# Optimization experiments

Measured on AMD Instinct MI355X. Metric: run time of the kernel, lower is better.

Reference implementation:

```python
import jax, jax.numpy as jnp
import numpy as np

B, L, P = 65536, 512, 96
E_LIN, E = 14, 16
FFT = 512
TEMP = 0.07
K = 2
EPS = 1e-5


def setup_inputs() -> dict:
    key = jax.random.key(0)
    k0, k1, k2 = jax.random.split(key, 3)
    x = jax.random.normal(k0, (B, L), dtype=jnp.float32)
    Wg = jax.random.normal(k1, (E, FFT // 2), dtype=jnp.float32) * 0.02
    bg = jnp.zeros((E,), dtype=jnp.float32)
    Wr = jax.random.normal(k2, (E_LIN, P, L), dtype=jnp.float32) * 0.02
    br = jnp.zeros((E_LIN, P), dtype=jnp.float32)
    return {"x": x, "Wg": Wg, "bg": bg, "Wr": Wr, "br": br}


def _periodogram(x):
    # x: [B, L] -> normalized power spectrum [B, FFT//2]
    x0 = x - jnp.mean(x, axis=1, keepdims=True)
    dft = jnp.fft.fft(x0, n=FFT, axis=1) / np.float32(np.sqrt(FFT))
    dft = dft[:, : FFT // 2]
    I = dft.real ** 2 + dft.imag ** 2
    s = jnp.sum(I, axis=1, keepdims=True)
    s = jnp.where(s == 0, jnp.ones_like(s), s)
    return I / s


def reference(x, Wg, bg, Wr, br):
    # gating (eval mode: no noise, divide by temperature)
    I = _periodogram(x)                                  # [B, F/2]
    gate = (I @ Wg.T + bg) / TEMP                        # [B, E]
    topv, topi = jax.lax.top_k(gate, K)                  # [B, K]
    gates = jax.nn.softmax(topv, axis=1)                 # [B, K]

    # RLinear experts: RevIN(norm) -> Linear -> RevIN(denorm); stats detached
    mu = jax.lax.stop_gradient(jnp.mean(x, axis=1, keepdims=True))        # [B,1]
    sd = jax.lax.stop_gradient(jnp.sqrt(jnp.var(x, axis=1, keepdims=True) + EPS))
    xn = (x - mu) / sd                                   # [B, L]
    yr = jnp.einsum('bl,epl->bep', xn, Wr) + br          # [B, E_LIN, P]
    yr = yr * sd[:, :, None] + mu[:, :, None]

    mean_out = jnp.broadcast_to(jnp.mean(x, axis=1, keepdims=True), (x.shape[0], P))[:, None, :]
    naive_out = jnp.broadcast_to(x[:, -1:], (x.shape[0], P))[:, None, :]

    eo = jnp.concatenate([yr, mean_out, naive_out], axis=1)   # [B, E, P]
    sel = jnp.take_along_axis(eo, topi[:, :, None], axis=1)   # [B, K, P]
    out = jnp.sum(gates[:, :, None] * sel, axis=1)            # [B, P]
    return out
```

## Files before the change

### kernel.cpp

```cpp
#include <hip/hip_runtime.h>
#include <math.h>

#define NB_B 65536
#define NL   512
#define NP   96
#define NE   16
#define NEL  14
#define NF   256
#define TEMP_INV (1.0f/0.07f)
#define TAU  1e-5f
#define PI_D 3.14159265358979323846
#define MAXCHK 1536

typedef __attribute__((ext_vector_type(8))) short bf16x8;
typedef __attribute__((ext_vector_type(4))) float f32x4;
typedef __attribute__((ext_vector_type(4))) unsigned int u32x4;


#define WS_PCNT     0
#define WS_HOLES    16384
#define WS_PBASE    32768
#define WS_FLAGCNT  33792
#define WS_NCHK     33824
#define WS_HOLECNT  33840
#define WS_FLAG     33856
#define WS_SSUM     296000
#define WS_WGT      301376
#define WS_BGT      317760
#define WS_TWD      319872
#define WS_REC      328064
#define WS_HDR      590208
#define WS_RIDX     1638784
#define WS_WRB      1933696
#define WS_DESC     3506560
#define WS_XB16     3512704
#define WS_XB16_END 70621568

__device__ __forceinline__ unsigned short f2bf(float f) {
    unsigned u = __float_as_uint(f);
    unsigned r = (u + 0x7fffu + ((u >> 16) & 1u)) >> 16;
    return (unsigned short)r;
}
__device__ __forceinline__ bf16x8 ldnt_bf16x8(const unsigned short* p) {
    u32x4 v = __builtin_nontemporal_load((const u32x4*)p);
    union { u32x4 u; bf16x8 h; } c; c.u = v; return c.h;
}
__device__ __forceinline__ float4 ldnt_f4(const float4* p) {
    u32x4 v = __builtin_nontemporal_load((const u32x4*)p);
    union { u32x4 u; float4 f; } c; c.u = v; return c.f;
}

__global__ __launch_bounds__(256) void k_prep(
    const float* __restrict__ Wg, const float* __restrict__ bg,
    const float* __restrict__ Wr,
    float* __restrict__ Ssum, float* __restrict__ WgE, float* __restrict__ bgT,
    double2* __restrict__ twd,
    int* __restrict__ pcnt, int* __restrict__ flagcnt, int* __restrict__ holecnt,
    ushort4* __restrict__ Wrb, int perm)
{
    int g = blockIdx.x * 256 + threadIdx.x;
    {
        ushort4 o = make_ushort4(0, 0, 0, 0);
        if (g < NEL * NP * NL / 4) {
            float4 v;
            if (perm) {
                int row = g >> 7, sq = g & 127;
                int ll = sq >> 1, kb = (sq & 1) * 4;
                const float* wr = Wr + (size_t)row * NL + ll;
                v.x = wr[(kb + 0) * 64]; v.y = wr[(kb + 1) * 64];
                v.z = wr[(kb + 2) * 64]; v.w = wr[(kb + 3) * 64];
            } else {
                v = ((const float4*)Wr)[g];
            }
            o.x = f2bf(v.x); o.y = f2bf(v.y); o.z = f2bf(v.z); o.w = f2bf(v.w);
        }
        Wrb[g] = o;
    }
    if (g < NEL * NP * 8) {
        int row = g >> 3, seg = g & 7;
        const float4* w = (const float4*)(Wr + (size_t)row * NL + seg * 64);
        float s = 0.f;
#pragma unroll
        for (int i = 0; i < 16; i++) { float4 v = w[i]; s += v.x + v.y + v.z + v.w; }
        s += __shfl_xor(s, 1); s += __shfl_xor(s, 2); s += __shfl_xor(s, 4);
        if (seg == 0) Ssum[row] = s;
    }
    if (g < 4096) {
        int c = g & 3, e = (g >> 2) & 15, f4 = g >> 6;
        WgE[g] = Wg[e * NF + f4 * 4 + c] * TEMP_INV;
    }
    if (g < 512) {
        double a = -2.0 * PI_D * (double)g / 512.0;
        twd[g] = make_double2(cos(a), sin(a));
    }
    if (g < 256) pcnt[g << 4] = 0;
    if (g < NE) bgT[g] = bg[g] * TEMP_INV;
    if (g == 300) *flagcnt = 0;
    if (g == 301) *holecnt = 0;
}

__global__ __launch_bounds__(256, 4) void k_gate(
    const float* __restrict__ x,
    const float4* __restrict__ WgE4, const float* __restrict__ bgT,
    int* __restrict__ rec, float4* __restrict__ hdr,
    int* __restrict__ flaglist, int* __restrict__ flagcnt,
    int* __restrict__ pcnt, unsigned short* __restrict__ xb16)
{
    __shared__ __align__(16) float2 s_z[4][576];
    float* s_Iv = (float*)&s_z[0][0];

    const int t = threadIdx.x;
    const int wv = t >> 6, l = t & 63;
    const int b0 = blockIdx.x * 8 + wv * 2;

    const float th = -6.283185307179586f / 512.0f;
    const float R2 = 0.70710678118654752f;
    float s1, c1; __sincosf((float)l * th, &s1, &c1);
    float s2, c2; __sincosf((float)(2 * l) * th, &s2, &c2);
    float sw0, cw0; __sincosf((float)((l & 31) << 3) * th, &sw0, &cw0);
    float sw1, cw1; __sincosf((float)((l & 15) << 4) * th, &sw1, &cw1);
    float sw2, cw2; __sincosf((float)((l & 7) << 5) * th, &sw2, &cw2);
    float2 tw0[4];
    tw0[0] = make_float2(c1, s1);
    tw0[1] = make_float2(R2 * (c1 + s1), R2 * (s1 - c1));
    tw0[2] = make_float2(s1, -c1);
    tw0[3] = make_float2(tw0[1].y, -tw0[1].x);
    float2 tw1[2];
    tw1[0] = make_float2(c2, s2);
    tw1[1] = make_float2(s2, -c2);
    const float2 w2 = make_float2(c2 * c2 - s2 * s2, 2.f * c2 * s2);
    float2 wst[5];
    wst[0] = make_float2(cw0, sw0);
    wst[1] = make_float2(cw1, sw1);
    wst[2] = make_float2(cw2, sw2);
    {
        int j2 = l & 3;
        float cc3 = (j2 == 0) ? 1.f : (j2 == 1) ? R2 : (j2 == 2) ? 0.f : -R2;
        float ss3 = (j2 == 0) ? 0.f : (j2 == 2) ? -1.f : -R2;
        wst[3] = make_float2(cc3, ss3);
    }
    wst[4] = (l & 1) ? make_float2(0.f, -1.f) : make_float2(1.f, 0.f);

    const float* xa = x + (size_t)b0 * NL;
    const float* xb = xa + NL;
    float xr[8], xi[8];
#pragma unroll
    for (int k = 0; k < 8; k++) { xr[k] = xa[k * 64 + l]; xi[k] = xb[k * 64 + l]; }
    const float last_a = __shfl(xr[7], 63);
    const float last_b = __shfl(xi[7], 63);

    if (xb16) {
        unsigned pa_[4], pb_[4];
#pragma unroll
        for (int j = 0; j < 4; j++) {
            asm("v_cvt_pk_bf16_f32 %0, %1, %2" : "=v"(pa_[j]) : "v"(xr[2 * j]), "v"(xr[2 * j + 1]));
            asm("v_cvt_pk_bf16_f32 %0, %1, %2" : "=v"(pb_[j]) : "v"(xi[2 * j]), "v"(xi[2 * j + 1]));
        }
        *(uint4*)(xb16 + (size_t)b0 * NL + l * 8)       = *(uint4*)pa_;
        *(uint4*)(xb16 + (size_t)(b0 + 1) * NL + l * 8) = *(uint4*)pb_;
    }

#pragma unroll
    for (int k = 0; k < 4; k++) {
        float2 w = tw0[k];
        float ur = xr[k], ui = xi[k], vr = xr[k + 4], vi = xi[k + 4];
        xr[k] = ur + vr; xi[k] = ui + vi;
        float dr = ur - vr, di = ui - vi;
        xr[k + 4] = dr * w.x - di * w.y; xi[k + 4] = dr * w.y + di * w.x;
    }
    {
        const int kk[4] = {0, 1, 4, 5};
#pragma unroll
        for (int g2 = 0; g2 < 4; g2++) {
            int k = kk[g2];
            float2 w = tw1[k & 1];
            float ur = xr[k], ui = xi[k], vr = xr[k + 2], vi = xi[k + 2];
            xr[k] = ur + vr; xi[k] = ui + vi;
            float dr = ur - vr, di = ui - vi;
            xr[k + 2] = dr * w.x - di * w.y; xi[k + 2] = dr * w.y + di * w.x;
        }
    }
    {
#pragma unroll
        for (int k = 0; k < 8; k += 2) {
            float ur = xr[k], ui = xi[k], vr = xr[k + 1], vi = xi[k + 1];
            xr[k] = ur + vr; xi[k] = ui + vi;
            float dr = ur - vr, di = ui - vi;
            xr[k + 1] = dr * w2.x - di * w2.y; xi[k + 1] = dr * w2.y + di * w2.x;
        }
    }
#pragma unroll
    for (int st = 3; st < 8; st++) {
        const int half = 256 >> st;
        const float2 w = wst[st - 3];
        const bool up = (l & half) != 0;
        const float sg = up ? -1.f : 1.f;
        const float cc = up ? w.x : 1.f;
        const float ss = up ? w.y : 0.f;
#pragma unroll
        for (int k = 0; k < 8; k++) {
            float pr = __shfl_xor(xr[k], half);
            float pi = __shfl_xor(xi[k], half);
            float tr = fmaf(sg, xr[k], pr);
            float ti = fmaf(sg, xi[k], pi);
            xr[k] = tr * cc - ti * ss;
            xi[k] = tr * ss + ti * cc;
        }
    }
    {
        const float sg = (l & 1) ? -1.f : 1.f;
#pragma unroll
        for (int k = 0; k < 8; k++) {
            float pr = __shfl_xor(xr[k], 1);
            float pi = __shfl_xor(xi[k], 1);
            xr[k] = fmaf(sg, xr[k], pr);
            xi[k] = fmaf(sg, xi[k], pi);
        }
    }

#pragma unroll
    for (int k = 0; k < 8; k++) {
        int i = k * 64 + l;
        s_z[wv][i + (i >> 3)] = make_float2(xr[k], xi[k]);
    }

    float Ia[4], Ib[4];
    float psa = 0.f, psb = 0.f;
#pragma unroll
    for (int j = 0; j < 4; j++) {
        int f = (l << 2) | j;
        int i1_ = (int)(__brev((unsigned)f) >> 23);
        int i2_ = (int)(__brev((unsigned)((512 - f) & 511)) >> 23);
        float2 z1 = s_z[wv][i1_ + (i1_ >> 3)];
        float2 z2 = s_z[wv][i2_ + (i2_ >> 3)];
        float pr_ = z1.x + z2.x, qm = z1.y - z2.y;
        float qp = z1.y + z2.y, pm = z1.x - z2.x;
        float va = pr_ * pr_ + qm * qm;
        float vb = qp * qp + pm * pm;
        if (f == 0) { va = 0.f; vb = 0.f; }
        Ia[j] = va; Ib[j] = vb;
        psa += va; psb += vb;
    }
#pragma unroll
    for (int m = 1; m < 64; m <<= 1) {
        psa += __shfl_xor(psa, m); psb += __shfl_xor(psb, m);
    }
    const float psa_raw = psa, psb_raw = psb;
    if (psa == 0.f) psa = 1.f;
    if (psb == 0.f) psb = 1.f;
    const float inv_a = 1.f / psa, inv_b = 1.f / psb;

    const float2 Z0   = s_z[wv][0];
    const float2 Z256 = s_z[wv][1];

    float* wI = s_Iv + wv * 1152;
    const int io = (l << 2) + ((l >> 4) << 2);
    *(float4*)(wI + io)       = make_float4(Ia[0], Ia[1], Ia[2], Ia[3]);
    *(float4*)(wI + 272 + io) = make_float4(Ib[0], Ib[1], Ib[2], Ib[3]);

    const int e16 = l & 15, cq = l >> 4;
    const float bgv = bgT[e16];
    float accA = 0.f, accB = 0.f;
    const float* rA = wI + cq * 68;
    const float* rB = rA + 272;
#pragma unroll 4
    for (int jj = 0; jj < 16; jj++) {
        float4 ia = *(const float4*)(rA + 4 * jj);
        float4 ib = *(const float4*)(rB + 4 * jj);
        float4 w = WgE4[(cq * 16 + jj) * 16 + e16];
        accA += ia.x * w.x + ia.y * w.y + ia.z * w.z + ia.w * w.w;
        accB += ib.x * w.x + ib.y * w.y + ib.z * w.z + ib.w * w.w;
    }
    accA += __shfl_xor(accA, 16); accA += __shfl_xor(accA, 32);
    accB += __shfl_xor(accB, 16); accB += __shfl_xor(accB, 32);

    float v = ((l & 16) ? accB * inv_b : accA * inv_a) + bgv;

    float b0v = v; int b0i = e16;
#pragma unroll
    for (int m = 1; m < 16; m <<= 1) {
        float ov = __shfl_xor(b0v, m); int oi = __shfl_xor(b0i, m);
        if (ov > b0v || (ov == b0v && oi < b0i)) { b0v = ov; b0i = oi; }
    }
    float v1 = (e16 == b0i) ? -1e30f : v;
    float b1v = v1; int b1i = e16;
#pragma unroll
    for (int m = 1; m < 16; m <<= 1) {
        float ov = __shfl_xor(b1v, m); int oi = __shfl_xor(b1i, m);
        if (ov > b1v || (ov == b1v && oi < b1i)) { b1v = ov; b1i = oi; }
    }
    float v2 = (e16 == b1i) ? -1e30f : v1;
    float b2v = v2;
#pragma unroll
    for (int m = 1; m < 16; m <<= 1) {
        float ov = __shfl_xor(b2v, m);
        b2v = fmaxf(b2v, ov);
    }

    if (l == 0 || l == 16) {
        const int r = l >> 4;
        const int b = b0 + r;
        const float mu = (r ? Z0.y : Z0.x) * (1.f / 512.f);
        const float Jv = r ? Z256.y : Z256.x;
        const float ps = r ? psb_raw : psa_raw;
        const float sd = sqrtf((0.5f * ps + Jv * Jv) * (1.f / 262144.f) + 1e-5f);
        const float last = r ? last_b : last_a;
        const float w0 = 1.f / (1.f + expf(b1v - b0v));
        const int pid = b0i * 16 + b1i;
        const int lo = atomicAdd(&pcnt[pid << 4], 1);
        rec[b] = (pid << 24) | lo;
        hdr[b] = make_float4(mu, sd, last, w0);
        if (b1v - b2v < TAU) {
            int pos = atomicAdd(flagcnt, 1);
            flaglist[pos] = b;
        }
    }
}

__global__ __launch_bounds__(256) void k_refine(
    const float* __restrict__ x, const double2* __restrict__ twd,
    const float* __restrict__ Wg, const float* __restrict__ bg,
    int* __restrict__ rec, float4* __restrict__ hdr,
    const int* __restrict__ flaglist, const int* __restrict__ flagcnt,
    int* __restrict__ pcnt, int* __restrict__ holes, int* __restrict__ holecnt)
{
    __shared__ double s_x[512];
    __shared__ double s_I[256];
    __shared__ double s_red[16];
    __shared__ double s_g[16];
    const int nf = *flagcnt;
    const int t = threadIdx.x;
    const int wid = t >> 6, lane = t & 63;
    for (int fi = blockIdx.x; fi < nf; fi += gridDim.x) {
        const int b = flaglist[fi];
        const float* xp = x + (size_t)b * NL;
        double v0 = (double)xp[t], v1 = (double)xp[t + 256];
        double lsum = v0 + v1;
        for (int m = 1; m < 64; m <<= 1) lsum += __shfl_xor(lsum, m);
        if (lane == 0) s_red[wid] = lsum;
        __syncthreads();
        double mu = (s_red[0] + s_red[1] + s_red[2] + s_red[3]) * (1.0 / 512.0);
        s_x[t] = v0 - mu; s_x[t + 256] = v1 - mu;
        __syncthreads();
        double2 w = twd[t];
        double pr = 1.0, pi = 0.0, cr = 0.0, ci = 0.0;
        for (int n = 0; n < 512; n++) {
            double xv = s_x[n];
            cr += xv * pr; ci += xv * pi;
            double t2 = pr * w.x - pi * w.y;
            pi = pr * w.y + pi * w.x;
            pr = t2;
        }
        double I = cr * cr + ci * ci;
        s_I[t] = I;
        double ls = I;
        for (int m = 1; m < 64; m <<= 1) ls += __shfl_xor(ls, m);
        if (lane == 0) s_red[8 + wid] = ls;
        __syncthreads();
        double stot = s_red[8] + s_red[9] + s_red[10] + s_red[11];
        if (stot == 0.0) stot = 1.0;
        if (t < 16) {
            double acc = 0.0;
            const float* wrow = Wg + t * NF;
            for (int f = 0; f < NF; f++) acc += s_I[f] * (double)wrow[f];
            s_g[t] = (acc / stot + (double)bg[t]) * (1.0 / 0.07);
        }
        __syncthreads();
        if (t == 0) {
            double c0 = -1e300, c1 = -1e300; int j0 = 0, j1 = 0;
            for (int i = 0; i < 16; i++) {
                double v = s_g[i];
                if (v > c0) { c1 = c0; j1 = j0; c0 = v; j0 = i; }
                else if (v > c1) { c1 = v; j1 = i; }
            }
            double e1 = exp(c1 - c0);
            float w0f = (float)(1.0 / (1.0 + e1));
            int newpid = j0 * 16 + j1;
            int oldrec = rec[b];
            int oldpid = (int)(((unsigned)oldrec) >> 24);
            if (newpid == oldpid) {
                ((float*)(hdr + b))[3] = w0f;
            } else {
                int pos = atomicAdd(holecnt, 1);
                if (pos < 4096) {
                    int nlo = atomicAdd(&pcnt[newpid << 4], 1);
                    rec[b] = (newpid << 24) | nlo;
                    holes[pos] = oldrec;
                    ((float*)(hdr + b))[3] = w0f;
                }
            }
        }
        __syncthreads();
    }
}

__global__ __launch_bounds__(256) void k_scan(
    const int* __restrict__ pcnt, int* __restrict__ pbase,
    int* __restrict__ desc, int* __restrict__ nchk)
{
    __shared__ int s[256], c[256];
    const int t = threadIdx.x;
    const int n = pcnt[t << 4];
    s[t] = n;
    c[t] = (n + 63) >> 6;
    __syncthreads();
    for (int off = 1; off < 256; off <<= 1) {
        int v1 = (t >= off) ? s[t - off] : 0;
        int v2 = (t >= off) ? c[t - off] : 0;
        __syncthreads();
        s[t] += v1; c[t] += v2;
        __syncthreads();
    }
    int excl = t ? s[t - 1] : 0;
    int cexcl = t ? c[t - 1] : 0;
    pbase[t] = excl;
    int myc = (n + 63) >> 6;
    for (int j = 0; j < myc; j++) desc[cexcl + j] = (t << 16) | j;
    if (t == 255) *nchk = cexcl + myc;
}

__global__ __launch_bounds__(256) void k_scatter(
    const int* __restrict__ rec, const int* __restrict__ pbase,
    int* __restrict__ ridx,
    const int* __restrict__ holes, const int* __restrict__ holecnt)
{
    const int t = threadIdx.x;
    const int b = blockIdx.x * 256 + t;
    unsigned v = (unsigned)rec[b];
    ridx[pbase[v >> 24] + (v & 0xFFFFFF)] = b;
    if (blockIdx.x == 0) {
        int nh = *holecnt; if (nh > 4096) nh = 4096;
        for (int h = t; h < nh; h += 256) {
            unsigned hv = (unsigned)holes[h];
            ridx[pbase[hv >> 24] + (hv & 0xFFFFFF)] = -1;
        }
    }
}

__global__ __launch_bounds__(256) void k_gemm3(
    const unsigned short* __restrict__ xb16,
    const unsigned short* __restrict__ Wrb,
    const float* __restrict__ br, const float* __restrict__ Ssum,
    const float4* __restrict__ hdr, float* __restrict__ out,
    const int* __restrict__ pcnt, const int* __restrict__ pbase,
    const int* __restrict__ ridx,
    const int* __restrict__ desc, const int* __restrict__ nchk)
{
    __shared__ __align__(16) unsigned short sB[2][96 * 68];
    __shared__ int    s_idx[64];
    __shared__ float4 s_hdr[64];
    __shared__ float  s_br[2][96], s_S[2][96];
    const int lb = (int)(blockIdx.x % 8) * (MAXCHK / 8) + (int)(blockIdx.x / 8);
    if (lb >= *nchk) return;
    const int d = desc[lb];
    const int pid = d >> 16, cc = d & 0xffff;
    const int n = pcnt[pid << 4];
    const int base = pbase[pid];
    const int i0 = pid >> 4, i1 = pid & 15;
    const int t = threadIdx.x;
    const int lane = t & 63, wv = t >> 6;
    const int quad = lane >> 4, l16 = lane & 15;
    if (t < 96) {
        s_br[0][t] = (i0 < NEL) ? br[i0 * NP + t] : 0.f;
        s_S [0][t] = (i0 < NEL) ? Ssum[i0 * NP + t] : 0.f;
        s_br[1][t] = (i1 < NEL) ? br[i1 * NP + t] : 0.f;
        s_S [1][t] = (i1 < NEL) ? Ssum[i1 * NP + t] : 0.f;
    }
    if (t < 64) {
        int g = cc * 64 + t;
        bool vld = g < n;
        int row = vld ? ridx[base + g] : -1;
        s_idx[t] = row;
        s_hdr[t] = (row >= 0) ? ldnt_f4(hdr + row) : make_float4(0.f, 0.f, 0.f, 0.f);
    }

    const unsigned short* wb[2];
    wb[0] = Wrb + (size_t)i0 * NP * NL;
    wb[1] = Wrb + (size_t)i1 * NP * NL;
    unsigned boff[6]; int bpos[6], bex[6];
#pragma unroll
    for (int it = 0; it < 6; it++) {
        int ex = (it >= 3);
        int fl = t + (it - 3 * ex) * 256;
        int p = fl >> 3, kg = fl & 7;
        bex[it] = ex;
        boff[it] = (unsigned)(p * NL + kg * 8);
        bpos[it] = p * 68 + kg * 8;
    }

    bf16x8 bR[6];
#pragma unroll
    for (int it = 0; it < 6; it++) bR[it] = *(const bf16x8*)(wb[bex[it]] + boff[it]);
    __syncthreads();

    int arow = s_idx[wv * 16 + l16]; if (arow < 0) arow = 0;
    const unsigned short* aP = xb16 + (size_t)arow * NL + quad * 8;

    f32x4 acc[2][6];
#pragma unroll
    for (int ex = 0; ex < 2; ex++)
#pragma unroll
        for (int j = 0; j < 6; j++) acc[ex][j] = (f32x4){0.f, 0.f, 0.f, 0.f};

    bf16x8 a0 = ldnt_bf16x8(aP);
    bf16x8 a1 = ldnt_bf16x8(aP + 32);

    for (int kb = 0; kb < NL; kb += 64) {
#pragma unroll
        for (int it = 0; it < 6; it++) *(bf16x8*)(&sB[bex[it]][bpos[it]]) = bR[it];
        __syncthreads();

        const int kn = kb + 64;
        bf16x8 an0, an1;
        if (kn < NL) {
#pragma unroll
            for (int it = 0; it < 6; it++)
                bR[it] = *(const bf16x8*)(wb[bex[it]] + boff[it] + kn);
            an0 = ldnt_bf16x8(aP + kn);
            an1 = ldnt_bf16x8(aP + kn + 32);
        }

#pragma unroll
        for (int ks = 0; ks < 2; ks++)
#pragma unroll
            for (int ex = 0; ex < 2; ex++)
#pragma unroll
                for (int nt = 0; nt < 6; nt++) {
                    bf16x8 bf = *(const bf16x8*)(&sB[ex][(nt * 16 + l16) * 68 + ks * 32 + quad * 8]);
                    acc[ex][nt] = __builtin_amdgcn_mfma_f32_16x16x32_bf16(
                        ks ? a1 : a0, bf, acc[ex][nt], 0, 0, 0);
                }
        if (kn < NL) {
            __syncthreads();
            a0 = an0; a1 = an1;
        }
    }

#pragma unroll
    for (int i = 0; i < 4; i++) {
        int rloc = wv * 16 + quad * 4 + i;
        int row = s_idx[rloc];
        if (row >= 0) {
            float4 h = s_hdr[rloc];
            float mu = h.x, sd = h.y, last = h.z, w0 = h.w, w1 = 1.f - w0;
            float* orow = out + (size_t)row * NP;
#pragma unroll
            for (int nt = 0; nt < 6; nt++) {
                int p = nt * 16 + l16;
                float v0 = (i0 < NEL) ? (mu + s_br[0][p] * sd - mu * s_S[0][p] + acc[0][nt][i])
                                      : (i0 == NEL ? mu : last);
                float v1 = (i1 < NEL) ? (mu + s_br[1][p] * sd - mu * s_S[1][p] + acc[1][nt][i])
                                      : (i1 == NEL ? mu : last);
                __builtin_nontemporal_store(w0 * v0 + w1 * v1, &orow[p]);
            }
        }
    }
}

__global__ __launch_bounds__(256) void k_gemm_f32(
    const float* __restrict__ x,
    const unsigned short* __restrict__ Wrb,
    const float* __restrict__ br, const float* __restrict__ Ssum,
    const float4* __restrict__ hdr, float* __restrict__ out,
    const int* __restrict__ pcnt, const int* __restrict__ pbase,
    const int* __restrict__ ridx,
    const int* __restrict__ desc, const int* __restrict__ nchk)
{
    __shared__ __align__(16) unsigned short sA[64 * 72];
    __shared__ __align__(16) unsigned short sB[2][96 * 72];
    __shared__ int    s_idx[64];
    __shared__ float4 s_hdr[64];
    __shared__ float  s_br[2][96], s_S[2][96];
    if ((int)blockIdx.x >= *nchk) return;
    const int d = desc[blockIdx.x];
    const int pid = d >> 16, cc = d & 0xffff;
    const int n = pcnt[pid << 4];
    const int base = pbase[pid];
    const int i0 = pid >> 4, i1 = pid & 15;
    const int t = threadIdx.x;
    const int lane = t & 63, wv = t >> 6;
    const int quad = lane >> 4, l16 = lane & 15;
    const int ar = t >> 2, asub = t & 3;
    if (t < 96) {
        s_br[0][t] = (i0 < NEL) ? br[i0 * NP + t] : 0.f;
        s_S [0][t] = (i0 < NEL) ? Ssum[i0 * NP + t] : 0.f;
        s_br[1][t] = (i1 < NEL) ? br[i1 * NP + t] : 0.f;
        s_S [1][t] = (i1 < NEL) ? Ssum[i1 * NP + t] : 0.f;
    }
    if (t < 64) {
        int g = cc * 64 + t;
        bool vld = g < n;
        int row = vld ? ridx[base + g] : -1;
        s_idx[t] = row;
        s_hdr[t] = (row >= 0) ? hdr[row] : make_float4(0.f, 0.f, 0.f, 0.f);
    }
    __syncthreads();

    f32x4 acc[2][6];
#pragma unroll
    for (int ex = 0; ex < 2; ex++)
#pragma unroll
        for (int j = 0; j < 6; j++) acc[ex][j] = (f32x4){0.f, 0.f, 0.f, 0.f};

    int rr = s_idx[ar]; if (rr < 0) rr = 0;

    unsigned boff[6];
    unsigned short* bdst[6];
    const unsigned short* wb[2];
    wb[0] = Wrb + (size_t)i0 * NP * NL;
    wb[1] = Wrb + (size_t)i1 * NP * NL;
    int bex[6];
#pragma unroll
    for (int it = 0; it < 6; it++) {
        int ex = (it >= 3);
        int fl = t + (it - 3 * ex) * 256;
        int p = fl >> 3, kg = fl & 7;
        bex[it] = ex;
        boff[it] = (unsigned)(p * NL + kg * 8);
        bdst[it] = &sB[ex][p * 72 + kg * 8];
    }
    unsigned short* adst = sA + ar * 72 + asub * 16;
    const float* xrowf = x + (size_t)rr * NL + asub * 16;

    float4 fA[4]; bf16x8 bR[6];
#pragma unroll
    for (int i = 0; i < 4; i++) fA[i] = ((const float4*)xrowf)[i];
#pragma unroll
    for (int it = 0; it < 6; it++) bR[it] = *(const bf16x8*)(wb[bex[it]] + boff[it]);

    for (int kb = 0; kb < NL; kb += 64) {
        unsigned short tmp[16];
#pragma unroll
        for (int i = 0; i < 4; i++) {
            float4 v = fA[i];
            tmp[i * 4 + 0] = f2bf(v.x); tmp[i * 4 + 1] = f2bf(v.y);
            tmp[i * 4 + 2] = f2bf(v.z); tmp[i * 4 + 3] = f2bf(v.w);
        }
        *(bf16x8*)adst       = *(bf16x8*)tmp;
        *(bf16x8*)(adst + 8) = *(bf16x8*)(tmp + 8);
#pragma unroll
        for (int it = 0; it < 6; it++) *(bf16x8*)bdst[it] = bR[it];
        __syncthreads();

        const int kn = kb + 64;
        if (kn < NL) {
#pragma unroll
            for (int i = 0; i < 4; i++) fA[i] = ((const float4*)(xrowf + kn))[i];
#pragma unroll
            for (int it = 0; it < 6; it++)
                bR[it] = *(const bf16x8*)(wb[bex[it]] + boff[it] + kn);
        }

#pragma unroll
        for (int ks = 0; ks < 2; ks++) {
            bf16x8 af = *(const bf16x8*)(sA + (wv * 16 + l16) * 72 + ks * 32 + quad * 8);
#pragma unroll
            for (int ex = 0; ex < 2; ex++)
#pragma unroll
                for (int nt = 0; nt < 6; nt++) {
                    bf16x8 bf = *(const bf16x8*)(&sB[ex][(nt * 16 + l16) * 72 + ks * 32 + quad * 8]);
                    acc[ex][nt] = __builtin_amdgcn_mfma_f32_16x16x32_bf16(af, bf, acc[ex][nt], 0, 0, 0);
                }
        }
        __syncthreads();
    }
#pragma unroll
    for (int i = 0; i < 4; i++) {
        int rloc = wv * 16 + quad * 4 + i;
        int row = s_idx[rloc];
        if (row >= 0) {
            float4 h = s_hdr[rloc];
            float mu = h.x, sd = h.y, last = h.z, w0 = h.w, w1 = 1.f - w0;
            float* orow = out + (size_t)row * NP;
#pragma unroll
            for (int nt = 0; nt < 6; nt++) {
                int p = nt * 16 + l16;
                float v0 = (i0 < NEL) ? (mu + s_br[0][p] * sd - mu * s_S[0][p] + acc[0][nt][i])
                                      : (i0 == NEL ? mu : last);
                float v1 = (i1 < NEL) ? (mu + s_br[1][p] * sd - mu * s_S[1][p] + acc[1][nt][i])
                                      : (i1 == NEL ? mu : last);
                orow[p] = w0 * v0 + w1 * v1;
            }
        }
    }
}

extern "C" void kernel_launch(void* const* d_in, const int* in_sizes, int n_in,
                              void* d_out, int out_size, void* d_ws, size_t ws_size,
                              hipStream_t stream)
{
    const float* x  = (const float*)d_in[0];
    const float* Wg = (const float*)d_in[1];
    const float* bg = (const float*)d_in[2];
    const float* Wr = (const float*)d_in[3];
    const float* br = (const float*)d_in[4];
    float* out = (float*)d_out;
    char* ws = (char*)d_ws;

    int*     pcnt     = (int*)(ws + WS_PCNT);
    int*     holes    = (int*)(ws + WS_HOLES);
    int*     pbase    = (int*)(ws + WS_PBASE);
    int*     flagcnt  = (int*)(ws + WS_FLAGCNT);
    int*     nchk     = (int*)(ws + WS_NCHK);
    int*     holecnt  = (int*)(ws + WS_HOLECNT);
    int*     flaglist = (int*)(ws + WS_FLAG);
    float*   Ssum     = (float*)(ws + WS_SSUM);
    float*   WgE      = (float*)(ws + WS_WGT);
    float*   bgT      = (float*)(ws + WS_BGT);
    double2* twd      = (double2*)(ws + WS_TWD);
    int*     rec      = (int*)(ws + WS_REC);
    float4*  hdr      = (float4*)(ws + WS_HDR);
    int*     ridx     = (int*)(ws + WS_RIDX);
    unsigned short* Wrb = (unsigned short*)(ws + WS_WRB);
    int*     desc     = (int*)(ws + WS_DESC);

    const int use_xb = (ws_size >= (size_t)WS_XB16_END);
    unsigned short* xb16 = use_xb ? (unsigned short*)(ws + WS_XB16) : (unsigned short*)0;

    k_prep<<<dim3(768), dim3(256), 0, stream>>>(Wg, bg, Wr, Ssum, WgE, bgT, twd,
                                                pcnt, flagcnt, holecnt,
                                                (ushort4*)Wrb, use_xb);
    k_gate<<<dim3(NB_B / 8), dim3(256), 0, stream>>>(x, (const float4*)WgE, bgT,
                                                     rec, hdr, flaglist, flagcnt, pcnt, xb16);
    k_refine<<<dim3(512), dim3(256), 0, stream>>>(x, twd, Wg, bg, rec, hdr,
                                                  flaglist, flagcnt, pcnt, holes, holecnt);
    k_scan<<<dim3(1), dim3(256), 0, stream>>>(pcnt, pbase, desc, nchk);
    k_scatter<<<dim3(NB_B / 256), dim3(256), 0, stream>>>(rec, pbase, ridx, holes, holecnt);
    if (use_xb)
        k_gemm3<<<dim3(MAXCHK), dim3(256), 0, stream>>>(xb16, Wrb, br, Ssum, hdr, out,
                                                        pcnt, pbase, ridx, desc, nchk);
    else
        k_gemm_f32<<<dim3(MAXCHK), dim3(256), 0, stream>>>(x, Wrb, br, Ssum, hdr, out,
                                                           pcnt, pbase, ridx, desc, nchk);
}
```

Baseline: 304.4 us.

## Pre-bucket bf16 rows into contiguous per-expert-pair slots before GEMM

Adds a k_bucket kernel that copies each row's bf16 activation and header into a contiguous slot ordered by expert-pair bucket. The GEMM then reads A rows with contiguous addressing instead of gathering through ridx. This removes the indirect, scattered row loads in the GEMM. In exchange it adds an extra full read and write pass over the bf16 activations and needs a larger workspace. The GEMM also drops its block-index remapping and the nontemporal loads.

```diff
diff --git a/kernel.cpp b/kernel.cpp
--- a/kernel.cpp
+++ b/kernel.cpp
@@ -11,6 +11,7 @@
 #define TAU  1e-5f
 #define PI_D 3.14159265358979323846
 #define MAXCHK 1536
+#define NSLOT 73728
 
 typedef __attribute__((ext_vector_type(8))) short bf16x8;
 typedef __attribute__((ext_vector_type(4))) float f32x4;
@@ -35,19 +36,14 @@
 #define WS_DESC     3506560
 #define WS_XB16     3512704
 #define WS_XB16_END 70621568
+#define WS_XBS      70621568
+#define WS_HDRS     146119040
+#define WS_FULL_END 147298688
 
 __device__ __forceinline__ unsigned short f2bf(float f) {
     unsigned u = __float_as_uint(f);
     unsigned r = (u + 0x7fffu + ((u >> 16) & 1u)) >> 16;
     return (unsigned short)r;
-}
-__device__ __forceinline__ bf16x8 ldnt_bf16x8(const unsigned short* p) {
-    u32x4 v = __builtin_nontemporal_load((const u32x4*)p);
-    union { u32x4 u; bf16x8 h; } c; c.u = v; return c.h;
-}
-__device__ __forceinline__ float4 ldnt_f4(const float4* p) {
-    u32x4 v = __builtin_nontemporal_load((const u32x4*)p);
-    union { u32x4 u; float4 f; } c; c.u = v; return c.f;
 }
 
 __global__ __launch_bounds__(256) void k_prep(
@@ -419,6 +415,33 @@
     if (t == 255) *nchk = cexcl + myc;
 }
 
+__global__ __launch_bounds__(256) void k_bucket(
+    const int* __restrict__ rec, const int* __restrict__ pbase,
+    const unsigned short* __restrict__ xb16, const float4* __restrict__ hdr,
+    unsigned short* __restrict__ xbs, float4* __restrict__ hdrs,
+    int* __restrict__ ridx,
+    const int* __restrict__ holes, const int* __restrict__ holecnt)
+{
+    const int t = threadIdx.x;
+    const int wv = t >> 6, l = t & 63;
+    const int b = blockIdx.x * 4 + wv;
+    unsigned v = (unsigned)rec[b];
+    const int slot = pbase[v >> 24] + (int)(v & 0xFFFFFF);
+    uint4 d = *(const uint4*)(xb16 + (size_t)b * NL + l * 8);
+    *(uint4*)(xbs + (size_t)slot * NL + l * 8) = d;
+    if (l == 0) {
+        hdrs[slot] = hdr[b];
+        ridx[slot] = b;
+    }
+    if (blockIdx.x == 0) {
+        int nh = *holecnt; if (nh > 4096) nh = 4096;
+        for (int h = t; h < nh; h += 256) {
+            unsigned hv = (unsigned)holes[h];
+            ridx[pbase[hv >> 24] + (int)(hv & 0xFFFFFF)] = -1;
+        }
+    }
+}
+
 __global__ __launch_bounds__(256) void k_scatter(
     const int* __restrict__ rec, const int* __restrict__ pbase,
     int* __restrict__ ridx,
@@ -437,11 +460,11 @@
     }
 }
 
-__global__ __launch_bounds__(256) void k_gemm3(
-    const unsigned short* __restrict__ xb16,
+__global__ __launch_bounds__(256) void k_gemm4(
+    const unsigned short* __restrict__ xbs,
     const unsigned short* __restrict__ Wrb,
     const float* __restrict__ br, const float* __restrict__ Ssum,
-    const float4* __restrict__ hdr, float* __restrict__ out,
+    const float4* __restrict__ hdrs, float* __restrict__ out,
     const int* __restrict__ pcnt, const int* __restrict__ pbase,
     const int* __restrict__ ridx,
     const int* __restrict__ desc, const int* __restrict__ nchk)
@@ -450,12 +473,12 @@
     __shared__ int    s_idx[64];
     __shared__ float4 s_hdr[64];
     __shared__ float  s_br[2][96], s_S[2][96];
-    const int lb = (int)(blockIdx.x % 8) * (MAXCHK / 8) + (int)(blockIdx.x / 8);
-    if (lb >= *nchk) return;
-    const int d = desc[lb];
+    if ((int)blockIdx.x >= *nchk) return;
+    const int d = desc[blockIdx.x];
     const int pid = d >> 16, cc = d & 0xffff;
     const int n = pcnt[pid << 4];
     const int base = pbase[pid];
+    const int slotbase = base + cc * 64;
     const int i0 = pid >> 4, i1 = pid & 15;
     const int t = threadIdx.x;
     const int lane = t & 63, wv = t >> 6;
@@ -467,11 +490,9 @@
         s_S [1][t] = (i1 < NEL) ? Ssum[i1 * NP + t] : 0.f;
     }
     if (t < 64) {
-        int g = cc * 64 + t;
-        bool vld = g < n;
-        int row = vld ? ridx[base + g] : -1;
-        s_idx[t] = row;
-        s_hdr[t] = (row >= 0) ? ldnt_f4(hdr + row) : make_float4(0.f, 0.f, 0.f, 0.f);
+        bool vld = (cc * 64 + t) < n;
+        s_idx[t] = vld ? ridx[slotbase + t] : -1;
+        s_hdr[t] = hdrs[slotbase + t];
     }
 
     const unsigned short* wb[2];
@@ -491,10 +512,8 @@
     bf16x8 bR[6];
 #pragma unroll
     for (int it = 0; it < 6; it++) bR[it] = *(const bf16x8*)(wb[bex[it]] + boff[it]);
-    __syncthreads();
-
-    int arow = s_idx[wv * 16 + l16]; if (arow < 0) arow = 0;
-    const unsigned short* aP = xb16 + (size_t)arow * NL + quad * 8;
+
+    const unsigned short* aP = xbs + (size_t)(slotbase + wv * 16 + l16) * NL + quad * 8;
 
     f32x4 acc[2][6];
 #pragma unroll
@@ -502,8 +521,8 @@
 #pragma unroll
         for (int j = 0; j < 6; j++) acc[ex][j] = (f32x4){0.f, 0.f, 0.f, 0.f};
 
-    bf16x8 a0 = ldnt_bf16x8(aP);
-    bf16x8 a1 = ldnt_bf16x8(aP + 32);
+    bf16x8 a0 = *(const bf16x8*)(aP);
+    bf16x8 a1 = *(const bf16x8*)(aP + 32);
 
     for (int kb = 0; kb < NL; kb += 64) {
 #pragma unroll
@@ -516,8 +535,8 @@
 #pragma unroll
             for (int it = 0; it < 6; it++)
                 bR[it] = *(const bf16x8*)(wb[bex[it]] + boff[it] + kn);
-            an0 = ldnt_bf16x8(aP + kn);
-            an1 = ldnt_bf16x8(aP + kn + 32);
+            an0 = *(const bf16x8*)(aP + kn);
+            an1 = *(const bf16x8*)(aP + kn + 32);
         }
 
 #pragma unroll
@@ -713,23 +732,30 @@
     int*     ridx     = (int*)(ws + WS_RIDX);
     unsigned short* Wrb = (unsigned short*)(ws + WS_WRB);
     int*     desc     = (int*)(ws + WS_DESC);
-
-    const int use_xb = (ws_size >= (size_t)WS_XB16_END);
-    unsigned short* xb16 = use_xb ? (unsigned short*)(ws + WS_XB16) : (unsigned short*)0;
+    unsigned short* xb16 = (unsigned short*)(ws + WS_XB16);
+    unsigned short* xbs  = (unsigned short*)(ws + WS_XBS);
+    float4*  hdrs     = (float4*)(ws + WS_HDRS);
+
+    const int use_full = (ws_size >= (size_t)WS_FULL_END);
+    const int use_xb   = use_full || (ws_size >= (size_t)WS_XB16_END);
 
     k_prep<<<dim3(768), dim3(256), 0, stream>>>(Wg, bg, Wr, Ssum, WgE, bgT, twd,
                                                 pcnt, flagcnt, holecnt,
                                                 (ushort4*)Wrb, use_xb);
     k_gate<<<dim3(NB_B / 8), dim3(256), 0, stream>>>(x, (const float4*)WgE, bgT,
-                                                     rec, hdr, flaglist, flagcnt, pcnt, xb16);
+                                                     rec, hdr, flaglist, flagcnt, pcnt,
+                                                     use_xb ? xb16 : (unsigned short*)0);
     k_refine<<<dim3(512), dim3(256), 0, stream>>>(x, twd, Wg, bg, rec, hdr,
                                                   flaglist, flagcnt, pcnt, holes, holecnt);
     k_scan<<<dim3(1), dim3(256), 0, stream>>>(pcnt, pbase, desc, nchk);
-    k_scatter<<<dim3(NB_B / 256), dim3(256), 0, stream>>>(rec, pbase, ridx, holes, holecnt);
-    if (use_xb)
-        k_gemm3<<<dim3(MAXCHK), dim3(256), 0, stream>>>(xb16, Wrb, br, Ssum, hdr, out,
+    if (use_full) {
+        k_bucket<<<dim3(NB_B / 4), dim3(256), 0, stream>>>(rec, pbase, xb16, hdr,
+                                                           xbs, hdrs, ridx, holes, holecnt);
+        k_gemm4<<<dim3(MAXCHK), dim3(256), 0, stream>>>(xbs, Wrb, br, Ssum, hdrs, out,
                                                         pcnt, pbase, ridx, desc, nchk);
-    else
+    } else {
+        k_scatter<<<dim3(NB_B / 256), dim3(256), 0, stream>>>(rec, pbase, ridx, holes, holecnt);
         k_gemm_f32<<<dim3(MAXCHK), dim3(256), 0, stream>>>(x, Wrb, br, Ssum, hdr, out,
                                                            pcnt, pbase, ridx, desc, nchk);
-}
+    }
+}
```

Result: slower. 324.1 us (+6.5%).
